# Kernel tuning notes

Hardware: AMD Instinct MI355X
Metric: run time of the kernel (lower is better)

## Reference

```python
import jax, jax.numpy as jnp
import numpy as np
import math

B, N = 1, 768
H, SQK, PQK, SV, PV = 12, 16, 4, 16, 8
CM, CP, COUT = 384, 128, 384
EPS = 1e-8
HUGE = 1e9


def setup_inputs() -> dict:
    key = jax.random.key(0)
    ks = jax.random.split(key, 12)
    rn = lambda k, shp, s=1.0: s * jax.random.normal(k, shp, jnp.float32)
    return {
        "inputs_1d": rn(ks[0], (B, N, CM)),
        "inputs_2d": rn(ks[1], (B, N, N, CP)),
        "mask": jnp.ones((B, N, 1), jnp.float32),
        "rot": rn(ks[2], (B, N, 3, 3)),
        "trans": rn(ks[3], (B, N, 3)),
        "wq": rn(ks[4], (CM, H * SQK), 0.05), "bq": jnp.zeros((H * SQK,), jnp.float32),
        "wkv": rn(ks[5], (CM, H * (SV + SQK)), 0.05), "bkv": jnp.zeros((H * (SV + SQK),), jnp.float32),
        "wqp": rn(ks[6], (CM, H * 3 * PQK), 0.05), "bqp": jnp.zeros((H * 3 * PQK,), jnp.float32),
        "wkvp": rn(ks[7], (CM, H * 3 * (PQK + PV)), 0.05), "bkvp": jnp.zeros((H * 3 * (PQK + PV),), jnp.float32),
        "w2d": rn(ks[8], (CP, H), 0.05), "b2d": jnp.zeros((H,), jnp.float32),
        "tpw": jnp.full((H,), 0.541323855, jnp.float32),
        "wout": rn(ks[9], (H * SV + H * PV * 4 + H * CP, COUT), 0.05),
        "bout": jnp.zeros((COUT,), jnp.float32),
    }


def reference(inputs_1d, inputs_2d, mask, rot, trans, wq, bq, wkv, bkv,
              wqp, bqp, wkvp, bkvp, w2d, b2d, tpw, wout, bout):
    # scalar q/k/v
    q_scalar = (inputs_1d @ wq + bq).reshape(B, N, H, SQK)
    kv_scalar = (inputs_1d @ wkv + bkv).reshape(B, N, H, SV + SQK)
    k_scalar, v_scalar = kv_scalar[..., :SQK], kv_scalar[..., SQK:]

    # point q/k/v in local frame, split into (x,y,z) chunks, map to global frame
    qp_local = (inputs_1d @ wqp + bqp).reshape(B, N, 3, H * PQK)
    qp_glob = jnp.einsum('bnij,bnjc->bnic', rot, qp_local) + trans[..., None]
    q_point = qp_glob.reshape(B, N, 3, H, PQK)

    kvp_local = (inputs_1d @ wkvp + bkvp).reshape(B, N, 3, H * (PQK + PV))
    kvp_glob = jnp.einsum('bnij,bnjc->bnic', rot, kvp_local) + trans[..., None]
    kvp_glob = kvp_glob.reshape(B, N, 3, H, PQK + PV)
    k_point, v_point = kvp_glob[..., :PQK], kvp_glob[..., PQK:]

    # logit weights
    scalar_weights = math.sqrt(1.0 / (3 * SQK))
    point_weights = math.sqrt(1.0 / (3 * PQK * 9.0 / 2)) * jax.nn.softplus(tpw)  # [H]
    attn2d_weights = math.sqrt(1.0 / 3)

    # point distance term: [B,H,N,PQK,3]
    qp = jnp.transpose(q_point, (0, 3, 1, 4, 2))
    kp = jnp.transpose(k_point, (0, 3, 1, 4, 2))
    dist2 = jnp.sum(jnp.square(qp[:, :, :, None] - kp[:, :, None]), axis=-1)  # [B,H,N,N,P]
    attn_qk_point = -0.5 * jnp.einsum('h,bhijp->bhij', point_weights, dist2)

    # scalar term
    q = scalar_weights * jnp.swapaxes(q_scalar, 1, 2)  # [B,H,N,SQK]
    k = jnp.swapaxes(k_scalar, 1, 2)
    attn_qk_scalar = jnp.einsum('bhqc,bhkc->bhqk', q, k)

    # pair bias
    attn_2d = jnp.transpose(inputs_2d @ w2d + b2d, (0, 3, 1, 2))  # [B,H,N,N]

    logits = attn_qk_scalar + attn_qk_point + attn2d_weights * attn_2d
    mask_2d = mask * jnp.swapaxes(mask, -1, -2)  # [B,N,N]
    logits = logits - HUGE * (1.0 - mask_2d[:, None])
    attn = jax.nn.softmax(logits, axis=-1)  # [B,H,N,N]

    # scalar values
    v = jnp.swapaxes(v_scalar, 1, 2)  # [B,H,N,SV]
    result_scalar = jnp.einsum('bhqk,bhkc->bqhc', attn, v).reshape(B, N, H * SV)

    # point values: [B,H,N,PV,3]
    vp = jnp.transpose(v_point, (0, 3, 1, 4, 2))
    rp = jnp.einsum('bhqk,bhkpd->bqhpd', attn, vp).reshape(B, N, H * PV, 3)
    rp_glob = jnp.transpose(rp, (0, 1, 3, 2))  # [B,N,3,H*PV]
    rp_local = jnp.einsum('bnji,bnjc->bnic', rot, rp_glob - trans[..., None])  # invert frame
    point_norm = jnp.sqrt(EPS + jnp.sum(jnp.square(rp_local), axis=2))  # [B,N,H*PV]

    # attention over pair features
    attn_over_2d = jnp.einsum('bhij,bijc->bihc', attn, inputs_2d).reshape(B, N, H * CP)

    final_act = jnp.concatenate(
        [result_scalar, rp_local[:, :, 0], rp_local[:, :, 1], rp_local[:, :, 2],
         point_norm, attn_over_2d], axis=-1)
    return final_act @ wout + bout
```

## Files before the change

### kernel.cpp

```cpp
#include <hip/hip_runtime.h>
#include <hip/hip_bf16.h>

#define NN 768
#define CM 384
#define FACT 2112

typedef __attribute__((ext_vector_type(8))) short bf16x8;
typedef __attribute__((ext_vector_type(4))) short bf16x4;
typedef __attribute__((ext_vector_type(4))) float f32x4;
typedef unsigned int u32;
typedef unsigned short u16;

__device__ __forceinline__ float bflo(u32 u){ union{u32 i; float f;} x; x.i = u << 16; return x.f; }
__device__ __forceinline__ float bfhi(u32 u){ union{u32 i; float f;} x; x.i = u & 0xffff0000u; return x.f; }
__device__ __forceinline__ u16 f2b(float f){ __hip_bfloat16 b = __float2bfloat16(f); return *(u16*)&b; }

__global__ __launch_bounds__(256) void k_proj(
    const float* __restrict__ in1d, const float* __restrict__ rot, const float* __restrict__ trans,
    const float* __restrict__ wq, const float* __restrict__ bq,
    const float* __restrict__ wkv, const float* __restrict__ bkv,
    const float* __restrict__ wqp, const float* __restrict__ bqp,
    const float* __restrict__ wkvp, const float* __restrict__ bkvp,
    float* __restrict__ qpack, u16* __restrict__ kpackb, u16* __restrict__ vpackb)
{
  const int n0 = blockIdx.x * 2;
  const int tid = threadIdx.x;
  __shared__ float x[2][CM];
  __shared__ float rs[2][9], ts[2][3];
  for (int idx = tid; idx < 2*CM; idx += 256)
    x[idx/CM][idx%CM] = in1d[(size_t)(n0 + idx/CM)*CM + idx%CM];
  if (tid < 18) rs[tid/9][tid%9] = rot[n0*9 + tid];
  if (tid < 6)  ts[tid/3][tid%3] = trans[n0*3 + tid];
  __syncthreads();
  for (int it = tid; it < 2*576; it += 256) {
    int r = it / 576, o = it % 576;
    const float* xr = x[r]; int n = n0 + r;
    if (o < 192) {
      float acc = bq[o];
      for (int c4 = 0; c4 < 96; ++c4) {
        float4 xv = *(const float4*)(xr + c4*4);
        const float* wp = wq + (size_t)c4*4*192 + o;
        acc += xv.x*wp[0] + xv.y*wp[192] + xv.z*wp[384] + xv.w*wp[576];
      }
      qpack[((size_t)n*12 + (o>>4))*28 + (o&15)] = acc;
    } else {
      int o2 = o - 192;
      float acc = bkv[o2];
      for (int c4 = 0; c4 < 96; ++c4) {
        float4 xv = *(const float4*)(xr + c4*4);
        const float* wp = wkv + (size_t)c4*4*384 + o2;
        acc += xv.x*wp[0] + xv.y*wp[384] + xv.z*wp[768] + xv.w*wp[1152];
      }
      int h = o2 >> 5, u = o2 & 31;
      if (u < 16) kpackb[((size_t)n*12 + h)*32 + u] = f2b(acc);
      else        vpackb[((size_t)h*NN + n)*40 + (u - 16)] = f2b(acc);
    }
  }
  for (int it = tid; it < 2*192; it += 256) {
    int r = it / 192, ch = it % 192;
    const float* xr = x[r];
    float l0, l1, l2; int h, u; bool isq;
    if (ch < 48) {
      l0 = bqp[ch]; l1 = bqp[48+ch]; l2 = bqp[96+ch];
      for (int c4 = 0; c4 < 96; ++c4) {
        float4 xv = *(const float4*)(xr + c4*4);
        const float* wp = wqp + (size_t)c4*4*144 + ch;
        l0 += xv.x*wp[0]  + xv.y*wp[144] + xv.z*wp[288] + xv.w*wp[432];
        l1 += xv.x*wp[48] + xv.y*wp[192] + xv.z*wp[336] + xv.w*wp[480];
        l2 += xv.x*wp[96] + xv.y*wp[240] + xv.z*wp[384] + xv.w*wp[528];
      }
      h = ch >> 2; u = ch & 3; isq = true;
    } else {
      int c2 = ch - 48;
      l0 = bkvp[c2]; l1 = bkvp[144+c2]; l2 = bkvp[288+c2];
      for (int c4 = 0; c4 < 96; ++c4) {
        float4 xv = *(const float4*)(xr + c4*4);
        const float* wp = wkvp + (size_t)c4*4*432 + c2;
        l0 += xv.x*wp[0]   + xv.y*wp[432] + xv.z*wp[864]  + xv.w*wp[1296];
        l1 += xv.x*wp[144] + xv.y*wp[576] + xv.z*wp[1008] + xv.w*wp[1440];
        l2 += xv.x*wp[288] + xv.y*wp[720] + xv.z*wp[1152] + xv.w*wp[1584];
      }
      h = c2 / 12; u = c2 % 12; isq = false;
    }
    float g0 = rs[r][0]*l0 + rs[r][1]*l1 + rs[r][2]*l2 + ts[r][0];
    float g1 = rs[r][3]*l0 + rs[r][4]*l1 + rs[r][5]*l2 + ts[r][1];
    float g2 = rs[r][6]*l0 + rs[r][7]*l1 + rs[r][8]*l2 + ts[r][2];
    int n = n0 + r;
    if (isq) {
      float* p = &qpack[((size_t)n*12 + h)*28 + 16 + u*3];
      p[0]=g0; p[1]=g1; p[2]=g2;
    } else if (u < 4) {
      u16* p = &kpackb[((size_t)n*12 + h)*32 + 16 + u*3];
      p[0]=f2b(g0); p[1]=f2b(g1); p[2]=f2b(g2);
    } else {
      u16* p = &vpackb[((size_t)h*NN + n)*40 + 16 + (u-4)*3];
      p[0]=f2b(g0); p[1]=f2b(g1); p[2]=f2b(g2);
    }
  }
}

__global__ __launch_bounds__(256) void k_fused(
    const float* __restrict__ in2d, const float* __restrict__ mask,
    const float* __restrict__ w2d, const float* __restrict__ b2d, const float* __restrict__ tpw,
    const float* __restrict__ qpack, const u16* __restrict__ kpackb, const u16* __restrict__ vpackb,
    const float* __restrict__ rot, const float* __restrict__ trans,
    float* __restrict__ fact)
{
  const int i = blockIdx.x;
  const int tid = threadIdx.x;
  const int lane = tid & 63, wave = tid >> 6;
  const int hcol = lane & 15, lg4 = lane >> 4;

  __shared__ u16 tile[64*128];
  __shared__ u16 tileT[128*64];
  __shared__ u16 pbuf[16*64];
  __shared__ float mterm_s[NN];
  __shared__ float redm[4][16];
  __shared__ float mrun_s[16], scl_s[16], sdiv[16];
  __shared__ float ovs[12*40];

  float q[28];
  #pragma unroll
  for (int c = 0; c < 28; ++c) q[c] = (hcol < 12) ? qpack[(size_t)i*336 + hcol*28 + c] : 0.f;
  float pw_c = (hcol < 12) ? 0.1360827635f * log1pf(expf(tpw[hcol])) : 0.f;
  float b2_c = (hcol < 12) ? b2d[hcol] : 0.f;
  const int hq = (hcol < 12) ? hcol : 0;

  const float mi = mask[i];
  for (int jx = tid; jx < NN; jx += 256) mterm_s[jx] = 1e9f * (1.f - mi * mask[jx]);
  if (tid < 16) mrun_s[tid] = -1e30f;

  bf16x8 wfrag[4];
  #pragma unroll
  for (int kk = 0; kk < 4; ++kk) {
    #pragma unroll
    for (int e = 0; e < 8; ++e) {
      int c = kk*32 + lg4*8 + e;
      float v = (hcol < 12) ? w2d[c*12 + hcol] : 0.f;
      wfrag[kk][e] = (short)f2b(v);
    }
  }

  f32x4 acc2[2] = {{0.f,0.f,0.f,0.f},{0.f,0.f,0.f,0.f}};
  float ovacc[3][8];
  #pragma unroll
  for (int hh = 0; hh < 3; ++hh)
    #pragma unroll
    for (int e = 0; e < 8; ++e) ovacc[hh][e] = 0.f;
  float s_c = 0.f;
  const int u8 = lane & 7, jp8 = lane >> 3;

  for (int t = 0; t < 12; ++t) {
    const int j0 = t*64;
    #pragma unroll
    for (int k = 0; k < 4; ++k) {
      int idx = tid + 256*k;
      int j = idx >> 4, cu = idx & 15;
      const float4* src = (const float4*)(in2d + ((size_t)i*NN + j0 + j)*128 + cu*8);
      float4 a = src[0], b = src[1];
      u16 hv[8] = { f2b(a.x),f2b(a.y),f2b(a.z),f2b(a.w), f2b(b.x),f2b(b.y),f2b(b.z),f2b(b.w) };
      bf16x8 pk;
      #pragma unroll
      for (int e = 0; e < 8; ++e) pk[e] = (short)hv[e];
      *(bf16x8*)&tile[j*128 + ((cu ^ (j&7))<<3)] = pk;
      int xj = j ^ ((cu & 7) << 3);
      #pragma unroll
      for (int e = 0; e < 8; ++e) tileT[(cu*8+e)*64 + xj] = hv[e];
    }
    __syncthreads();
    const int jA = wave*16 + hcol;
    f32x4 bias = {0.f,0.f,0.f,0.f};
    #pragma unroll
    for (int kk = 0; kk < 4; ++kk) {
      bf16x8 a = *(const bf16x8*)&tile[jA*128 + ((((kk<<2)|lg4) ^ (jA&7))<<3)];
      bias = __builtin_amdgcn_mfma_f32_16x16x32_bf16(a, wfrag[kk], bias, 0, 0, 0);
    }
    float lgt[4];
    #pragma unroll
    for (int r = 0; r < 4; ++r) {
      int jl = wave*16 + lg4*4 + r;
      int j = j0 + jl;
      const uint4* kr = (const uint4*)(kpackb + ((size_t)j*12 + hq)*32);
      float qk = 0.f;
      #pragma unroll
      for (int kk = 0; kk < 2; ++kk) {
        uint4 u = kr[kk];
        const float* qp = &q[kk*8];
        qk += qp[0]*bflo(u.x) + qp[1]*bfhi(u.x) + qp[2]*bflo(u.y) + qp[3]*bfhi(u.y)
            + qp[4]*bflo(u.z) + qp[5]*bfhi(u.z) + qp[6]*bflo(u.w) + qp[7]*bfhi(u.w);
      }
      float pt = 0.f;
      {
        uint4 u = kr[2]; float d;
        d = q[16]-bflo(u.x); pt += d*d;  d = q[17]-bfhi(u.x); pt += d*d;
        d = q[18]-bflo(u.y); pt += d*d;  d = q[19]-bfhi(u.y); pt += d*d;
        d = q[20]-bflo(u.z); pt += d*d;  d = q[21]-bfhi(u.z); pt += d*d;
        d = q[22]-bflo(u.w); pt += d*d;  d = q[23]-bfhi(u.w); pt += d*d;
        uint2 u2 = *(const uint2*)(((const u32*)kr) + 12);
        d = q[24]-bflo(u2.x); pt += d*d; d = q[25]-bfhi(u2.x); pt += d*d;
        d = q[26]-bflo(u2.y); pt += d*d; d = q[27]-bfhi(u2.y); pt += d*d;
      }
      lgt[r] = 0.1443375673f*qk - 0.5f*pw_c*pt + 0.5773502692f*(bias[r] + b2_c) - mterm_s[j];
    }
    float mx = fmaxf(fmaxf(lgt[0], lgt[1]), fmaxf(lgt[2], lgt[3]));
    mx = fmaxf(mx, __shfl_xor(mx, 16));
    mx = fmaxf(mx, __shfl_xor(mx, 32));
    if (lane < 16) redm[wave][lane] = mx;
    __syncthreads();
    if (tid < 16) {
      float mt = fmaxf(fmaxf(redm[0][tid], redm[1][tid]), fmaxf(redm[2][tid], redm[3][tid]));
      float mo = mrun_s[tid];
      float mn = fmaxf(mo, mt);
      scl_s[tid] = __expf(mo - mn);
      mrun_s[tid] = mn;
    }
    __syncthreads();
    {
      float mn_c = mrun_s[hcol];
      float p0 = __expf(lgt[0]-mn_c), p1 = __expf(lgt[1]-mn_c);
      float p2 = __expf(lgt[2]-mn_c), p3 = __expf(lgt[3]-mn_c);
      s_c = s_c * scl_s[hcol] + (p0+p1+p2+p3);
      int jb = wave*16 + lg4*4;
      bf16x4 pv;
      pv[0]=(short)f2b(p0); pv[1]=(short)f2b(p1); pv[2]=(short)f2b(p2); pv[3]=(short)f2b(p3);
      *(bf16x4*)&pbuf[hcol*64 + (((jb>>3) ^ (hcol&7))<<3) + (jb&7)] = pv;
    }
    #pragma unroll
    for (int r = 0; r < 4; ++r) {
      float s = scl_s[lg4*4 + r];
      acc2[0][r] *= s; acc2[1][r] *= s;
    }
    #pragma unroll
    for (int hh = 0; hh < 3; ++hh) {
      float s = scl_s[wave + 4*hh];
      #pragma unroll
      for (int e = 0; e < 8; ++e) ovacc[hh][e] *= s;
    }
    __syncthreads();
    bf16x8 pf[2];
    #pragma unroll
    for (int ks = 0; ks < 2; ++ks) {
      int jb = ks*32 + lg4*8;
      pf[ks] = *(const bf16x8*)&pbuf[hcol*64 + (((jb>>3) ^ (hcol&7))<<3)];
    }
    #pragma unroll
    for (int cb = 0; cb < 2; ++cb) {
      int cc = (wave*2 + cb)*16 + hcol;
      #pragma unroll
      for (int ks = 0; ks < 2; ++ks) {
        int J = ks*32 + lg4*8;
        bf16x8 b = *(const bf16x8*)&tileT[cc*64 + (J ^ (((cc>>3)&7)<<3))];
        acc2[cb] = __builtin_amdgcn_mfma_f32_16x16x32_bf16(pf[ks], b, acc2[cb], 0, 0, 0);
      }
    }
    if (u8 < 5) {
      #pragma unroll
      for (int hh = 0; hh < 3; ++hh) {
        int h2 = wave + 4*hh;
        #pragma unroll
        for (int jj = 0; jj < 8; ++jj) {
          int j = jj*8 + jp8;
          float p = bflo((u32)pbuf[h2*64 + ((jj ^ (h2&7))<<3) + jp8]);
          uint4 u = *(const uint4*)(vpackb + ((size_t)h2*NN + j0 + j)*40 + u8*8);
          ovacc[hh][0] += p*bflo(u.x); ovacc[hh][1] += p*bfhi(u.x);
          ovacc[hh][2] += p*bflo(u.y); ovacc[hh][3] += p*bfhi(u.y);
          ovacc[hh][4] += p*bflo(u.z); ovacc[hh][5] += p*bfhi(u.z);
          ovacc[hh][6] += p*bflo(u.w); ovacc[hh][7] += p*bfhi(u.w);
        }
      }
    }
    __syncthreads();
  }

  s_c += __shfl_xor(s_c, 16);
  s_c += __shfl_xor(s_c, 32);
  if (lane < 16) redm[wave][lane] = s_c;
  __syncthreads();
  if (tid < 16) sdiv[tid] = 1.f / (redm[0][tid] + redm[1][tid] + redm[2][tid] + redm[3][tid]);
  __syncthreads();
  #pragma unroll
  for (int cb = 0; cb < 2; ++cb) {
    int c = (wave*2 + cb)*16 + hcol;
    #pragma unroll
    for (int r = 0; r < 4; ++r) {
      int h = lg4*4 + r;
      if (h < 12)
        fact[(size_t)i*FACT + 576 + (size_t)h*128 + c] = acc2[cb][r] * sdiv[h];
    }
  }
  #pragma unroll
  for (int hh = 0; hh < 3; ++hh)
    #pragma unroll
    for (int e = 0; e < 8; ++e) {
      ovacc[hh][e] += __shfl_xor(ovacc[hh][e], 8);
      ovacc[hh][e] += __shfl_xor(ovacc[hh][e], 16);
      ovacc[hh][e] += __shfl_xor(ovacc[hh][e], 32);
    }
  if (lane < 5) {
    #pragma unroll
    for (int hh = 0; hh < 3; ++hh) {
      int h2 = wave + 4*hh;
      float inv = sdiv[h2];
      #pragma unroll
      for (int e = 0; e < 8; ++e) ovs[h2*40 + lane*8 + e] = ovacc[hh][e] * inv;
    }
  }
  __syncthreads();
  if (tid < 192) {
    int h = tid >> 4, c = tid & 15;
    fact[(size_t)i*FACT + h*16 + c] = ovs[h*40 + c];
  }
  if (tid < 96) {
    int h = tid >> 3, p = tid & 7;
    float g0 = ovs[h*40 + 16 + 3*p + 0] - trans[i*3+0];
    float g1 = ovs[h*40 + 16 + 3*p + 1] - trans[i*3+1];
    float g2 = ovs[h*40 + 16 + 3*p + 2] - trans[i*3+2];
    const float* R = rot + i*9;
    float l0 = R[0]*g0 + R[3]*g1 + R[6]*g2;
    float l1 = R[1]*g0 + R[4]*g1 + R[7]*g2;
    float l2 = R[2]*g0 + R[5]*g1 + R[8]*g2;
    size_t base = (size_t)i*FACT;
    fact[base + 192 +   0 + h*8 + p] = l0;
    fact[base + 192 +  96 + h*8 + p] = l1;
    fact[base + 192 + 192 + h*8 + p] = l2;
    fact[base + 480 + h*8 + p] = sqrtf(1e-8f + l0*l0 + l1*l1 + l2*l2);
  }
}

#define KCH 704
__global__ __launch_bounds__(256) void k_out_part(
    const float* __restrict__ fact, const float* __restrict__ wout, float* __restrict__ pout)
{
  const int r0 = blockIdx.x * 16;
  const int c0 = blockIdx.y * 64;
  const int kc = blockIdx.z;
  __shared__ float xs[16][64];
  const int tid = threadIdx.x;
  const int co = tid & 63, rg = tid >> 6;
  float acc[4] = {0.f,0.f,0.f,0.f};
  for (int ks = 0; ks < 11; ++ks) {
    int k0 = kc*KCH + ks*64;
    for (int idx = tid; idx < 1024; idx += 256) {
      int rr = idx >> 6, kx = idx & 63;
      xs[rr][kx] = fact[(size_t)(r0+rr)*FACT + k0 + kx];
    }
    __syncthreads();
    for (int kk = 0; kk < 64; ++kk) {
      float w = wout[(size_t)(k0+kk)*384 + c0 + co];
      acc[0] += xs[rg*4+0][kk]*w;
      acc[1] += xs[rg*4+1][kk]*w;
      acc[2] += xs[rg*4+2][kk]*w;
      acc[3] += xs[rg*4+3][kk]*w;
    }
    __syncthreads();
  }
  #pragma unroll
  for (int r = 0; r < 4; ++r)
    pout[((size_t)kc*NN + r0 + rg*4 + r)*384 + c0 + co] = acc[r];
}

__global__ __launch_bounds__(256) void k_out_red(
    const float* __restrict__ pout, const float* __restrict__ bout, float* __restrict__ out)
{
  int idx = blockIdx.x*256 + threadIdx.x;
  out[idx] = bout[idx % 384] + pout[idx] + pout[294912 + idx] + pout[2*294912 + idx];
}

extern "C" void kernel_launch(void* const* d_in, const int* in_sizes, int n_in,
                              void* d_out, int out_size, void* d_ws, size_t ws_size,
                              hipStream_t stream) {
  const float* in1d  = (const float*)d_in[0];
  const float* in2d  = (const float*)d_in[1];
  const float* mask  = (const float*)d_in[2];
  const float* rot   = (const float*)d_in[3];
  const float* trans = (const float*)d_in[4];
  const float* wq    = (const float*)d_in[5];
  const float* bq    = (const float*)d_in[6];
  const float* wkv   = (const float*)d_in[7];
  const float* bkv   = (const float*)d_in[8];
  const float* wqp   = (const float*)d_in[9];
  const float* bqp   = (const float*)d_in[10];
  const float* wkvp  = (const float*)d_in[11];
  const float* bkvp  = (const float*)d_in[12];
  const float* w2d   = (const float*)d_in[13];
  const float* b2d   = (const float*)d_in[14];
  const float* tpw   = (const float*)d_in[15];
  const float* wout  = (const float*)d_in[16];
  const float* bout  = (const float*)d_in[17];

  float* ws = (float*)d_ws;
  float* qpack  = ws;
  u16*   kpackb = (u16*)(ws + 258048);
  u16*   vpackb = (u16*)(ws + 405504);
  float* fact   = ws + 589824;
  float* pout   = ws + 2211840;
  float* out    = (float*)d_out;

  k_proj   <<<384, 256, 0, stream>>>(in1d, rot, trans, wq, bq, wkv, bkv, wqp, bqp,
                                     wkvp, bkvp, qpack, kpackb, vpackb);
  k_fused  <<<768, 256, 0, stream>>>(in2d, mask, w2d, b2d, tpw, qpack, kpackb, vpackb,
                                     rot, trans, fact);
  k_out_part<<<dim3(48,6,3), 256, 0, stream>>>(fact, wout, pout);
  k_out_red <<<1152, 256, 0, stream>>>(pout, bout, out);
}
```

Baseline: 296.8 us.

## Prefetch pair tiles into registers, double-buffer transpose, and trim fused-kernel syncs

The fused attention kernel now loads the next 64-row pair tile into registers while the current tile is processed. It double-buffers the transposed shared tile, which removes the trailing barrier and merges the softmax max update into every thread, dropping one barrier per iteration. It also switches to packed f32x2 math for the q·k, point-distance and value accumulation, computes the mask term inline instead of staging it in shared memory, and sets a 3-blocks-per-CU occupancy hint. The output GEMM processes 32 rows per block instead of 16 to reuse weight loads, at the cost of more registers and fewer blocks.

```diff
diff --git a/kernel.cpp b/kernel.cpp
--- a/kernel.cpp
+++ b/kernel.cpp
@@ -8,11 +8,16 @@
 typedef __attribute__((ext_vector_type(8))) short bf16x8;
 typedef __attribute__((ext_vector_type(4))) short bf16x4;
 typedef __attribute__((ext_vector_type(4))) float f32x4;
+typedef __attribute__((ext_vector_type(2))) float f32x2;
 typedef unsigned int u32;
 typedef unsigned short u16;
 
 __device__ __forceinline__ float bflo(u32 u){ union{u32 i; float f;} x; x.i = u << 16; return x.f; }
-__device__ __forceinline__ float bfhi(u32 u){ union{u32 i; float f;} x; x.i = u & 0xffff0000u; return x.f; }
+__device__ __forceinline__ f32x2 bfp(u32 u){
+  union { u32 i[2]; f32x2 v; } x;
+  x.i[0] = u << 16; x.i[1] = u & 0xffff0000u;
+  return x.v;
+}
 __device__ __forceinline__ u16 f2b(float f){ __hip_bfloat16 b = __float2bfloat16(f); return *(u16*)&b; }
 
 __global__ __launch_bounds__(256) void k_proj(
@@ -99,7 +104,7 @@
   }
 }
 
-__global__ __launch_bounds__(256) void k_fused(
+__global__ __launch_bounds__(256, 3) void k_fused(
     const float* __restrict__ in2d, const float* __restrict__ mask,
     const float* __restrict__ w2d, const float* __restrict__ b2d, const float* __restrict__ tpw,
     const float* __restrict__ qpack, const u16* __restrict__ kpackb, const u16* __restrict__ vpackb,
@@ -110,121 +115,148 @@
   const int tid = threadIdx.x;
   const int lane = tid & 63, wave = tid >> 6;
   const int hcol = lane & 15, lg4 = lane >> 4;
-
-  __shared__ u16 tile[64*128];
-  __shared__ u16 tileT[128*64];
-  __shared__ u16 pbuf[16*64];
-  __shared__ float mterm_s[NN];
+  const int jq = tid >> 4, cu = tid & 15;
+
+  __shared__ __align__(16) u16 tileJ[64*128];
+  __shared__ __align__(16) u16 tileT[2][128*64];
+  __shared__ __align__(16) u16 pbuf[16*64];
   __shared__ float redm[4][16];
-  __shared__ float mrun_s[16], scl_s[16], sdiv[16];
+  __shared__ float scl_s[16], sdiv[16];
   __shared__ float ovs[12*40];
 
-  float q[28];
-  #pragma unroll
-  for (int c = 0; c < 28; ++c) q[c] = (hcol < 12) ? qpack[(size_t)i*336 + hcol*28 + c] : 0.f;
-  float pw_c = (hcol < 12) ? 0.1360827635f * log1pf(expf(tpw[hcol])) : 0.f;
-  float b2_c = (hcol < 12) ? b2d[hcol] : 0.f;
+  f32x2 q2[14];
+  #pragma unroll
+  for (int c = 0; c < 14; ++c) {
+    if (hcol < 12) {
+      q2[c].x = qpack[(size_t)i*336 + hcol*28 + 2*c];
+      q2[c].y = qpack[(size_t)i*336 + hcol*28 + 2*c + 1];
+    } else { q2[c].x = 0.f; q2[c].y = 0.f; }
+  }
+  const float pw_c = (hcol < 12) ? 0.1360827635f * log1pf(expf(tpw[hcol])) : 0.f;
+  const float b2_c = (hcol < 12) ? b2d[hcol] : 0.f;
   const int hq = (hcol < 12) ? hcol : 0;
-
   const float mi = mask[i];
-  for (int jx = tid; jx < NN; jx += 256) mterm_s[jx] = 1e9f * (1.f - mi * mask[jx]);
-  if (tid < 16) mrun_s[tid] = -1e30f;
 
   bf16x8 wfrag[4];
   #pragma unroll
-  for (int kk = 0; kk < 4; ++kk) {
+  for (int kk = 0; kk < 4; ++kk)
     #pragma unroll
     for (int e = 0; e < 8; ++e) {
       int c = kk*32 + lg4*8 + e;
-      float v = (hcol < 12) ? w2d[c*12 + hcol] : 0.f;
-      wfrag[kk][e] = (short)f2b(v);
-    }
-  }
+      wfrag[kk][e] = (short)((hcol < 12) ? f2b(w2d[c*12 + hcol]) : (u16)0);
+    }
 
   f32x4 acc2[2] = {{0.f,0.f,0.f,0.f},{0.f,0.f,0.f,0.f}};
-  float ovacc[3][8];
+  f32x2 ovacc[3][4];
   #pragma unroll
   for (int hh = 0; hh < 3; ++hh)
     #pragma unroll
-    for (int e = 0; e < 8; ++e) ovacc[hh][e] = 0.f;
-  float s_c = 0.f;
+    for (int m = 0; m < 4; ++m) { ovacc[hh][m].x = 0.f; ovacc[hh][m].y = 0.f; }
+  float m_run = -1e30f, s_c = 0.f;
   const int u8 = lane & 7, jp8 = lane >> 3;
 
+  float4 pfr[8];
+  {
+    const float4* src = (const float4*)(in2d + (size_t)i*NN*128);
+    #pragma unroll
+    for (int r = 0; r < 4; ++r) {
+      pfr[2*r]   = src[(jq*4+r)*32 + cu*2];
+      pfr[2*r+1] = src[(jq*4+r)*32 + cu*2 + 1];
+    }
+  }
+
   for (int t = 0; t < 12; ++t) {
+    const int buf = t & 1;
     const int j0 = t*64;
-    #pragma unroll
-    for (int k = 0; k < 4; ++k) {
-      int idx = tid + 256*k;
-      int j = idx >> 4, cu = idx & 15;
-      const float4* src = (const float4*)(in2d + ((size_t)i*NN + j0 + j)*128 + cu*8);
-      float4 a = src[0], b = src[1];
-      u16 hv[8] = { f2b(a.x),f2b(a.y),f2b(a.z),f2b(a.w), f2b(b.x),f2b(b.y),f2b(b.z),f2b(b.w) };
-      bf16x8 pk;
-      #pragma unroll
-      for (int e = 0; e < 8; ++e) pk[e] = (short)hv[e];
-      *(bf16x8*)&tile[j*128 + ((cu ^ (j&7))<<3)] = pk;
-      int xj = j ^ ((cu & 7) << 3);
-      #pragma unroll
-      for (int e = 0; e < 8; ++e) tileT[(cu*8+e)*64 + xj] = hv[e];
+    u16* tt = (u16*)tileT[buf];
+    {
+      u16 hb[4][8];
+      #pragma unroll
+      for (int r = 0; r < 4; ++r) {
+        hb[r][0]=f2b(pfr[2*r].x);   hb[r][1]=f2b(pfr[2*r].y);
+        hb[r][2]=f2b(pfr[2*r].z);   hb[r][3]=f2b(pfr[2*r].w);
+        hb[r][4]=f2b(pfr[2*r+1].x); hb[r][5]=f2b(pfr[2*r+1].y);
+        hb[r][6]=f2b(pfr[2*r+1].z); hb[r][7]=f2b(pfr[2*r+1].w);
+      }
+      #pragma unroll
+      for (int r = 0; r < 4; ++r) {
+        int j = jq*4 + r;
+        bf16x8 pk;
+        #pragma unroll
+        for (int e = 0; e < 8; ++e) pk[e] = (short)hb[r][e];
+        *(bf16x8*)&tileJ[j*128 + ((cu ^ (j&7))<<3)] = pk;
+      }
+      #pragma unroll
+      for (int e = 0; e < 8; ++e) {
+        int c = cu*8 + e;
+        bf16x4 pv;
+        pv[0]=(short)hb[0][e]; pv[1]=(short)hb[1][e]; pv[2]=(short)hb[2][e]; pv[3]=(short)hb[3][e];
+        *(bf16x4*)&tt[c*64 + ((jq*4) ^ (((c&7) ^ ((c>>3)&7))<<3))] = pv;
+      }
+    }
+    if (t < 11) {
+      const float4* src = (const float4*)(in2d + ((size_t)i*NN + j0 + 64)*128);
+      #pragma unroll
+      for (int r = 0; r < 4; ++r) {
+        pfr[2*r]   = src[(jq*4+r)*32 + cu*2];
+        pfr[2*r+1] = src[(jq*4+r)*32 + cu*2 + 1];
+      }
     }
     __syncthreads();
+
     const int jA = wave*16 + hcol;
     f32x4 bias = {0.f,0.f,0.f,0.f};
     #pragma unroll
     for (int kk = 0; kk < 4; ++kk) {
-      bf16x8 a = *(const bf16x8*)&tile[jA*128 + ((((kk<<2)|lg4) ^ (jA&7))<<3)];
+      bf16x8 a = *(const bf16x8*)&tileJ[jA*128 + ((((kk<<2)|lg4) ^ (jA&7))<<3)];
       bias = __builtin_amdgcn_mfma_f32_16x16x32_bf16(a, wfrag[kk], bias, 0, 0, 0);
     }
+
     float lgt[4];
     #pragma unroll
     for (int r = 0; r < 4; ++r) {
-      int jl = wave*16 + lg4*4 + r;
-      int j = j0 + jl;
+      int j = j0 + wave*16 + lg4*4 + r;
       const uint4* kr = (const uint4*)(kpackb + ((size_t)j*12 + hq)*32);
-      float qk = 0.f;
-      #pragma unroll
-      for (int kk = 0; kk < 2; ++kk) {
-        uint4 u = kr[kk];
-        const float* qp = &q[kk*8];
-        qk += qp[0]*bflo(u.x) + qp[1]*bfhi(u.x) + qp[2]*bflo(u.y) + qp[3]*bfhi(u.y)
-            + qp[4]*bflo(u.z) + qp[5]*bfhi(u.z) + qp[6]*bflo(u.w) + qp[7]*bfhi(u.w);
-      }
-      float pt = 0.f;
-      {
-        uint4 u = kr[2]; float d;
-        d = q[16]-bflo(u.x); pt += d*d;  d = q[17]-bfhi(u.x); pt += d*d;
-        d = q[18]-bflo(u.y); pt += d*d;  d = q[19]-bfhi(u.y); pt += d*d;
-        d = q[20]-bflo(u.z); pt += d*d;  d = q[21]-bfhi(u.z); pt += d*d;
-        d = q[22]-bflo(u.w); pt += d*d;  d = q[23]-bfhi(u.w); pt += d*d;
-        uint2 u2 = *(const uint2*)(((const u32*)kr) + 12);
-        d = q[24]-bflo(u2.x); pt += d*d; d = q[25]-bfhi(u2.x); pt += d*d;
-        d = q[26]-bflo(u2.y); pt += d*d; d = q[27]-bfhi(u2.y); pt += d*d;
-      }
-      lgt[r] = 0.1443375673f*qk - 0.5f*pw_c*pt + 0.5773502692f*(bias[r] + b2_c) - mterm_s[j];
-    }
+      uint4 ka = kr[0], kb = kr[1], kc2 = kr[2];
+      uint2 kd = ((const uint2*)kr)[6];
+      float mj = mask[j];
+      f32x2 qk2 = q2[0]*bfp(ka.x);
+      qk2 += q2[1]*bfp(ka.y); qk2 += q2[2]*bfp(ka.z); qk2 += q2[3]*bfp(ka.w);
+      qk2 += q2[4]*bfp(kb.x); qk2 += q2[5]*bfp(kb.y); qk2 += q2[6]*bfp(kb.z); qk2 += q2[7]*bfp(kb.w);
+      f32x2 d, pt2;
+      d = q2[8]  - bfp(kc2.x); pt2  = d*d;
+      d = q2[9]  - bfp(kc2.y); pt2 += d*d;
+      d = q2[10] - bfp(kc2.z); pt2 += d*d;
+      d = q2[11] - bfp(kc2.w); pt2 += d*d;
+      d = q2[12] - bfp(kd.x);  pt2 += d*d;
+      d = q2[13] - bfp(kd.y);  pt2 += d*d;
+      lgt[r] = 0.1443375673f*(qk2.x+qk2.y) - 0.5f*pw_c*(pt2.x+pt2.y)
+             + 0.5773502692f*(bias[r] + b2_c) - 1e9f*(1.f - mi*mj);
+    }
+
     float mx = fmaxf(fmaxf(lgt[0], lgt[1]), fmaxf(lgt[2], lgt[3]));
     mx = fmaxf(mx, __shfl_xor(mx, 16));
     mx = fmaxf(mx, __shfl_xor(mx, 32));
     if (lane < 16) redm[wave][lane] = mx;
     __syncthreads();
-    if (tid < 16) {
-      float mt = fmaxf(fmaxf(redm[0][tid], redm[1][tid]), fmaxf(redm[2][tid], redm[3][tid]));
-      float mo = mrun_s[tid];
-      float mn = fmaxf(mo, mt);
-      scl_s[tid] = __expf(mo - mn);
-      mrun_s[tid] = mn;
-    }
-    __syncthreads();
+
+    float mt = fmaxf(fmaxf(redm[0][hcol], redm[1][hcol]), fmaxf(redm[2][hcol], redm[3][hcol]));
+    float mn = fmaxf(m_run, mt);
+    float scl = __expf(m_run - mn);
+    m_run = mn;
+    if (tid < 16) scl_s[tid] = scl;
+
+    float p0 = __expf(lgt[0]-mn), p1 = __expf(lgt[1]-mn);
+    float p2v = __expf(lgt[2]-mn), p3 = __expf(lgt[3]-mn);
+    s_c = s_c*scl + (p0+p1+p2v+p3);
     {
-      float mn_c = mrun_s[hcol];
-      float p0 = __expf(lgt[0]-mn_c), p1 = __expf(lgt[1]-mn_c);
-      float p2 = __expf(lgt[2]-mn_c), p3 = __expf(lgt[3]-mn_c);
-      s_c = s_c * scl_s[hcol] + (p0+p1+p2+p3);
       int jb = wave*16 + lg4*4;
       bf16x4 pv;
-      pv[0]=(short)f2b(p0); pv[1]=(short)f2b(p1); pv[2]=(short)f2b(p2); pv[3]=(short)f2b(p3);
+      pv[0]=(short)f2b(p0); pv[1]=(short)f2b(p1); pv[2]=(short)f2b(p2v); pv[3]=(short)f2b(p3);
       *(bf16x4*)&pbuf[hcol*64 + (((jb>>3) ^ (hcol&7))<<3) + (jb&7)] = pv;
     }
+    __syncthreads();
+
     #pragma unroll
     for (int r = 0; r < 4; ++r) {
       float s = scl_s[lg4*4 + r];
@@ -233,43 +265,39 @@
     #pragma unroll
     for (int hh = 0; hh < 3; ++hh) {
       float s = scl_s[wave + 4*hh];
-      #pragma unroll
-      for (int e = 0; e < 8; ++e) ovacc[hh][e] *= s;
-    }
-    __syncthreads();
-    bf16x8 pf[2];
-    #pragma unroll
-    for (int ks = 0; ks < 2; ++ks) {
-      int jb = ks*32 + lg4*8;
-      pf[ks] = *(const bf16x8*)&pbuf[hcol*64 + (((jb>>3) ^ (hcol&7))<<3)];
-    }
+      ovacc[hh][0] *= s; ovacc[hh][1] *= s; ovacc[hh][2] *= s; ovacc[hh][3] *= s;
+    }
+
+    bf16x8 pf0 = *(const bf16x8*)&pbuf[hcol*64 + ((lg4 ^ (hcol&7))<<3)];
+    bf16x8 pf1 = *(const bf16x8*)&pbuf[hcol*64 + (((4 + lg4) ^ (hcol&7))<<3)];
     #pragma unroll
     for (int cb = 0; cb < 2; ++cb) {
-      int cc = (wave*2 + cb)*16 + hcol;
-      #pragma unroll
-      for (int ks = 0; ks < 2; ++ks) {
-        int J = ks*32 + lg4*8;
-        bf16x8 b = *(const bf16x8*)&tileT[cc*64 + (J ^ (((cc>>3)&7)<<3))];
-        acc2[cb] = __builtin_amdgcn_mfma_f32_16x16x32_bf16(pf[ks], b, acc2[cb], 0, 0, 0);
-      }
-    }
+      int c = (wave*2 + cb)*16 + hcol;
+      int swz = ((c&7) ^ ((c>>3)&7)) << 3;
+      const u16* tb = &tt[c*64];
+      bf16x8 b0 = *(const bf16x8*)&tb[(lg4*8) ^ swz];
+      acc2[cb] = __builtin_amdgcn_mfma_f32_16x16x32_bf16(pf0, b0, acc2[cb], 0, 0, 0);
+      bf16x8 b1 = *(const bf16x8*)&tb[(32 + lg4*8) ^ swz];
+      acc2[cb] = __builtin_amdgcn_mfma_f32_16x16x32_bf16(pf1, b1, acc2[cb], 0, 0, 0);
+    }
+
     if (u8 < 5) {
       #pragma unroll
       for (int hh = 0; hh < 3; ++hh) {
-        int h2 = wave + 4*hh;
+        const int h2 = wave + 4*hh;
         #pragma unroll
         for (int jj = 0; jj < 8; ++jj) {
           int j = jj*8 + jp8;
           float p = bflo((u32)pbuf[h2*64 + ((jj ^ (h2&7))<<3) + jp8]);
+          f32x2 p2 = {p, p};
           uint4 u = *(const uint4*)(vpackb + ((size_t)h2*NN + j0 + j)*40 + u8*8);
-          ovacc[hh][0] += p*bflo(u.x); ovacc[hh][1] += p*bfhi(u.x);
-          ovacc[hh][2] += p*bflo(u.y); ovacc[hh][3] += p*bfhi(u.y);
-          ovacc[hh][4] += p*bflo(u.z); ovacc[hh][5] += p*bfhi(u.z);
-          ovacc[hh][6] += p*bflo(u.w); ovacc[hh][7] += p*bfhi(u.w);
+          ovacc[hh][0] += p2*bfp(u.x);
+          ovacc[hh][1] += p2*bfp(u.y);
+          ovacc[hh][2] += p2*bfp(u.z);
+          ovacc[hh][3] += p2*bfp(u.w);
         }
       }
     }
-    __syncthreads();
   }
 
   s_c += __shfl_xor(s_c, 16);
@@ -288,13 +316,18 @@
         fact[(size_t)i*FACT + 576 + (size_t)h*128 + c] = acc2[cb][r] * sdiv[h];
     }
   }
+  float ove[3][8];
   #pragma unroll
   for (int hh = 0; hh < 3; ++hh)
     #pragma unroll
+    for (int m = 0; m < 4; ++m) { ove[hh][2*m] = ovacc[hh][m].x; ove[hh][2*m+1] = ovacc[hh][m].y; }
+  #pragma unroll
+  for (int hh = 0; hh < 3; ++hh)
+    #pragma unroll
     for (int e = 0; e < 8; ++e) {
-      ovacc[hh][e] += __shfl_xor(ovacc[hh][e], 8);
-      ovacc[hh][e] += __shfl_xor(ovacc[hh][e], 16);
-      ovacc[hh][e] += __shfl_xor(ovacc[hh][e], 32);
+      ove[hh][e] += __shfl_xor(ove[hh][e], 8);
+      ove[hh][e] += __shfl_xor(ove[hh][e], 16);
+      ove[hh][e] += __shfl_xor(ove[hh][e], 32);
     }
   if (lane < 5) {
     #pragma unroll
@@ -302,7 +335,7 @@
       int h2 = wave + 4*hh;
       float inv = sdiv[h2];
       #pragma unroll
-      for (int e = 0; e < 8; ++e) ovs[h2*40 + lane*8 + e] = ovacc[hh][e] * inv;
+      for (int e = 0; e < 8; ++e) ovs[h2*40 + lane*8 + e] = ove[hh][e] * inv;
     }
   }
   __syncthreads();
@@ -327,36 +360,33 @@
   }
 }
 
-#define KCH 704
 __global__ __launch_bounds__(256) void k_out_part(
     const float* __restrict__ fact, const float* __restrict__ wout, float* __restrict__ pout)
 {
-  const int r0 = blockIdx.x * 16;
+  const int r0 = blockIdx.x * 32;
   const int c0 = blockIdx.y * 64;
   const int kc = blockIdx.z;
-  __shared__ float xs[16][64];
+  __shared__ float xs[32][64];
   const int tid = threadIdx.x;
   const int co = tid & 63, rg = tid >> 6;
-  float acc[4] = {0.f,0.f,0.f,0.f};
+  float acc[8] = {0.f,0.f,0.f,0.f,0.f,0.f,0.f,0.f};
   for (int ks = 0; ks < 11; ++ks) {
-    int k0 = kc*KCH + ks*64;
-    for (int idx = tid; idx < 1024; idx += 256) {
+    int k0 = kc*704 + ks*64;
+    for (int idx = tid; idx < 2048; idx += 256) {
       int rr = idx >> 6, kx = idx & 63;
       xs[rr][kx] = fact[(size_t)(r0+rr)*FACT + k0 + kx];
     }
     __syncthreads();
     for (int kk = 0; kk < 64; ++kk) {
       float w = wout[(size_t)(k0+kk)*384 + c0 + co];
-      acc[0] += xs[rg*4+0][kk]*w;
-      acc[1] += xs[rg*4+1][kk]*w;
-      acc[2] += xs[rg*4+2][kk]*w;
-      acc[3] += xs[rg*4+3][kk]*w;
+      #pragma unroll
+      for (int rr = 0; rr < 8; ++rr) acc[rr] += xs[rg*8+rr][kk]*w;
     }
     __syncthreads();
   }
   #pragma unroll
-  for (int r = 0; r < 4; ++r)
-    pout[((size_t)kc*NN + r0 + rg*4 + r)*384 + c0 + co] = acc[r];
+  for (int rr = 0; rr < 8; ++rr)
+    pout[((size_t)kc*NN + r0 + rg*8 + rr)*384 + c0 + co] = acc[rr];
 }
 
 __global__ __launch_bounds__(256) void k_out_red(
@@ -400,6 +430,6 @@
                                      wkvp, bkvp, qpack, kpackb, vpackb);
   k_fused  <<<768, 256, 0, stream>>>(in2d, mask, w2d, b2d, tpw, qpack, kpackb, vpackb,
                                      rot, trans, fact);
-  k_out_part<<<dim3(48,6,3), 256, 0, stream>>>(fact, wout, pout);
+  k_out_part<<<dim3(24,6,3), 256, 0, stream>>>(fact, wout, pout);
   k_out_red <<<1152, 256, 0, stream>>>(pout, bout, out);
 }
```

Result: slower. 786.3 us (+165.0%).
